# Kernel tuning notes

Measured on AMD Instinct MI355X. Metric: run time of the kernel, lower is better.

The kernel has to match this reference:

```python
import jax, jax.numpy as jnp
import numpy as np

N = 100000          # nodes
E = 1_600_000       # edges (before self loops)
IN = 128            # in_channels
HID = 64            # hidden
HEADS = 4
EPS = 1e-5          # BatchNorm eps
NEG_SLOPE = 0.2     # GATConv leaky_relu slope


def setup_inputs() -> dict:
    key = jax.random.key(0)
    ks = jax.random.split(key, 16)
    he = lambda fan: (2.0 / fan) ** 0.5  # kaiming-normal scale
    d = {
        "x": jax.random.normal(ks[0], (N, IN), jnp.float32),
        "edge_index": jax.random.randint(ks[1], (2, E), 0, N, dtype=jnp.int64),
        "root_index": 0,
        "W1": jax.random.normal(ks[2], (IN, HEADS * HID), jnp.float32) * he(IN),
        "att_src1": jax.random.normal(ks[3], (HEADS, HID), jnp.float32) * 0.1,
        "att_dst1": jax.random.normal(ks[4], (HEADS, HID), jnp.float32) * 0.1,
        "b1": jnp.zeros((HEADS * HID,), jnp.float32),
        "W2": jax.random.normal(ks[5], (HEADS * HID, HID), jnp.float32) * he(HEADS * HID),
        "att_src2": jax.random.normal(ks[6], (1, HID), jnp.float32) * 0.1,
        "att_dst2": jax.random.normal(ks[7], (1, HID), jnp.float32) * 0.1,
        "b2": jnp.zeros((HID,), jnp.float32),
        "bn1_g": jnp.ones((HEADS * HID,), jnp.float32),
        "bn1_b": jnp.zeros((HEADS * HID,), jnp.float32),
        "bn1_m": jnp.zeros((HEADS * HID,), jnp.float32),
        "bn1_v": jnp.ones((HEADS * HID,), jnp.float32),
        "bn2_g": jnp.ones((HID,), jnp.float32),
        "bn2_b": jnp.zeros((HID,), jnp.float32),
        "bn2_m": jnp.zeros((HID,), jnp.float32),
        "bn2_v": jnp.ones((HID,), jnp.float32),
        "cg1_w": jax.random.normal(ks[8], (3 * HID, 64), jnp.float32) * he(3 * HID),
        "cg1_b": jnp.zeros((64,), jnp.float32),
        "cbn_g": jnp.ones((64,), jnp.float32),
        "cbn_b": jnp.zeros((64,), jnp.float32),
        "cbn_m": jnp.zeros((64,), jnp.float32),
        "cbn_v": jnp.ones((64,), jnp.float32),
        "cg2_w": jax.random.normal(ks[9], (64, 32), jnp.float32) * he(64),
        "cg2_b": jnp.zeros((32,), jnp.float32),
        "cg3_w": jax.random.normal(ks[10], (32, 1), jnp.float32) * he(32),
        "cg3_b": jnp.zeros((1,), jnp.float32),
    }
    return d


def _bn_eval(x, g, b, m, v):
    return (x - m) * jax.lax.rsqrt(v + EPS) * g + b


def _gat_conv(x, src, dst, W, att_src, att_dst, bias, heads, out_ch, concat):
    """PyG GATConv (eval mode, self loops already in src/dst)."""
    n = x.shape[0]
    h = (x @ W).reshape(n, heads, out_ch)                # [N,H,C]
    a_src = jnp.einsum('nhc,hc->nh', h, att_src)         # [N,H]
    a_dst = jnp.einsum('nhc,hc->nh', h, att_dst)
    e = jax.nn.leaky_relu(a_src[src] + a_dst[dst], NEG_SLOPE)   # [Etot,H]
    seg_max = jax.ops.segment_max(e, dst, num_segments=n)
    ex = jnp.exp(e - seg_max[dst])
    denom = jax.ops.segment_sum(ex, dst, num_segments=n)
    alpha = ex / (denom[dst] + 1e-16)                    # [Etot,H]
    msg = h[src] * alpha[:, :, None]                     # [Etot,H,C]
    out = jax.ops.segment_sum(msg, dst, num_segments=n)  # [N,H,C]
    if concat:
        return out.reshape(n, heads * out_ch) + bias
    return out.mean(axis=1) + bias


def reference(x, edge_index, root_index, W1, att_src1, att_dst1, b1,
              W2, att_src2, att_dst2, b2,
              bn1_g, bn1_b, bn1_m, bn1_v, bn2_g, bn2_b, bn2_m, bn2_v,
              cg1_w, cg1_b, cbn_g, cbn_b, cbn_m, cbn_v,
              cg2_w, cg2_b, cg3_w, cg3_b):
    n = x.shape[0]
    # add self loops (PyG GATConv default)
    loop = jnp.arange(n, dtype=edge_index.dtype)
    src = jnp.concatenate([edge_index[0], loop])
    dst = jnp.concatenate([edge_index[1], loop])

    h = _gat_conv(x, src, dst, W1, att_src1, att_dst1, b1, HEADS, HID, True)
    h = jax.nn.elu(_bn_eval(h, bn1_g, bn1_b, bn1_m, bn1_v))
    h = _gat_conv(h, src, dst, W2, att_src2, att_dst2, b2, 1, HID, False)
    node_emb = jax.nn.elu(_bn_eval(h, bn2_g, bn2_b, bn2_m, bn2_v))  # [N,HID]

    mean_emb = node_emb.mean(axis=0, keepdims=True)      # [1,HID]
    max_emb = node_emb.max(axis=0, keepdims=True)        # [1,HID]
    safe_root = min(root_index, n - 1)
    root_emb = node_emb[safe_root][None, :]              # single graph path
    g = jnp.concatenate([mean_emb, max_emb, root_emb], axis=-1)  # [1,3*HID]

    g = jax.nn.relu(_bn_eval(g @ cg1_w + cg1_b, cbn_g, cbn_b, cbn_m, cbn_v))
    g = jax.nn.relu(g @ cg2_w + cg2_b)
    logit = (g @ cg3_w + cg3_b).squeeze(-1)              # [1]
    return logit
```

## Files before the change

kernel.cpp:

```cpp
#include <hip/hip_runtime.h>

#define N_NODES 100000
#define N_EDGES 1600000
#define ETOT    1700000
#define IN_CH   128
#define C1      256
#define HID     64
#define BN_EPS  1e-5f
#define SLOPE   0.2f
#define NCHUNK  98
#define FILL_PH 8
#define PH_NODES 12500

typedef __attribute__((ext_vector_type(8))) short s16x8;
typedef __attribute__((ext_vector_type(4))) float f32x4;
#define MFMA16(a, b, c) __builtin_amdgcn_mfma_f32_16x16x32_bf16(a, b, c, 0, 0, 0)

__device__ __forceinline__ float leaky(float x) { return fmaxf(x, SLOPE * x); }
__device__ __forceinline__ float elu_f(float x) { return x > 0.f ? x : __expf(x) - 1.f; }
__device__ __forceinline__ unsigned short f2bf(float f) {
  unsigned int b = __float_as_uint(f);
  return (unsigned short)((b + 0x7FFFu + ((b >> 16) & 1u)) >> 16);
}
__device__ __forceinline__ float bf2f(unsigned short u) {
  return __uint_as_float((unsigned int)u << 16);
}

__global__ void __launch_bounds__(256) k_init_deg(int* __restrict__ deg) {
  int n = blockIdx.x * 256 + threadIdx.x;
  if (n < N_NODES) deg[n] = 1;
}

__global__ void __launch_bounds__(256) k_deg_ph(const int* __restrict__ edge, int* __restrict__ deg) {
  int bpp = (N_EDGES + 1023) >> 10;
  int ph = blockIdx.x / bpp;
  int lo = ph * PH_NODES, hi = lo + PH_NODES;
  int i0 = (blockIdx.x % bpp) * 1024 + threadIdx.x * 4;
  if (i0 >= N_EDGES) return;
  if (i0 + 3 < N_EDGES) {
    int4 dv = *(const int4*)(edge + N_EDGES + i0);
    if (dv.x >= lo && dv.x < hi) atomicAdd(&deg[dv.x], 1);
    if (dv.y >= lo && dv.y < hi) atomicAdd(&deg[dv.y], 1);
    if (dv.z >= lo && dv.z < hi) atomicAdd(&deg[dv.z], 1);
    if (dv.w >= lo && dv.w < hi) atomicAdd(&deg[dv.w], 1);
  } else {
    for (int j = 0; j < 4 && i0 + j < N_EDGES; j++) {
      int d = edge[N_EDGES + i0 + j];
      if (d >= lo && d < hi) atomicAdd(&deg[d], 1);
    }
  }
}

__global__ void __launch_bounds__(256) k_scan_part(const int* __restrict__ deg, int* __restrict__ part) {
  __shared__ int ls[256];
  int t = threadIdx.x;
  int base = blockIdx.x * 1024 + t * 4;
  int s = 0;
#pragma unroll
  for (int j = 0; j < 4; j++) if (base + j < N_NODES) s += deg[base + j];
  ls[t] = s;
  __syncthreads();
  for (int off = 128; off >= 1; off >>= 1) {
    if (t < off) ls[t] += ls[t + off];
    __syncthreads();
  }
  if (t == 0) part[blockIdx.x] = ls[0];
}

__global__ void k_scan_top(int* __restrict__ part, int* __restrict__ row_ptr) {
  if (threadIdx.x == 0 && blockIdx.x == 0) {
    int run = 0;
    for (int i = 0; i < NCHUNK; i++) { int t = part[i]; part[i] = run; run += t; }
    row_ptr[N_NODES] = run;
  }
}

__global__ void __launch_bounds__(256) k_scan_down(const int* __restrict__ deg, const int* __restrict__ part,
                                                   int* __restrict__ row_ptr, int* __restrict__ cursor) {
  __shared__ int ls[256];
  int t = threadIdx.x;
  int base = blockIdx.x * 1024 + t * 4;
  int v[4];
#pragma unroll
  for (int j = 0; j < 4; j++) v[j] = (base + j < N_NODES) ? deg[base + j] : 0;
  int tsum = v[0] + v[1] + v[2] + v[3];
  ls[t] = tsum;
  __syncthreads();
  for (int off = 1; off < 256; off <<= 1) {
    int add = (t >= off) ? ls[t - off] : 0;
    __syncthreads();
    ls[t] += add;
    __syncthreads();
  }
  int excl = ls[t] - tsum + part[blockIdx.x];
#pragma unroll
  for (int j = 0; j < 4; j++) {
    int idx = base + j;
    if (idx < N_NODES) { row_ptr[idx] = excl; cursor[idx] = excl; }
    excl += v[j];
  }
}

__global__ void __launch_bounds__(256) k_fill_ph(const int* __restrict__ edge, int* __restrict__ cursor,
                                                 int* __restrict__ col) {
  int bpp = (ETOT + 255) >> 8;
  int ph = blockIdx.x / bpp;
  int lo = ph * PH_NODES, hi = lo + PH_NODES;
  int i = (blockIdx.x % bpp) * 256 + threadIdx.x;
  if (i >= ETOT) return;
  int d = (i < N_EDGES) ? edge[N_EDGES + i] : (i - N_EDGES);
  if (d < lo || d >= hi) return;
  int s = (i < N_EDGES) ? edge[i] : d;
  int pos = atomicAdd(&cursor[d], 1);
  col[pos] = s;
}

__global__ void __launch_bounds__(256) k_prep(const float* __restrict__ W1, const float* __restrict__ W2,
                                              unsigned short* __restrict__ W1T, unsigned short* __restrict__ W2T) {
  int i = blockIdx.x * 256 + threadIdx.x;
  if (i < IN_CH * C1) {
    int k = i >> 8, c = i & 255;
    W1T[c * IN_CH + k] = f2bf(W1[i]);
  }
  if (i < C1 * HID) {
    int k = i >> 6, c = i & 63;
    W2T[c * C1 + k] = f2bf(W2[i]);
  }
}

__global__ void __launch_bounds__(256) k_gemm1(const float* __restrict__ x, const unsigned short* __restrict__ W1T,
                                               const float* __restrict__ attS, const float* __restrict__ attD,
                                               unsigned short* __restrict__ h1b, float* __restrict__ aS,
                                               float* __restrict__ aD) {
  __shared__ unsigned short As[64][IN_CH + 8];
  int tid = threadIdx.x;
  int w = tid >> 6, lane = tid & 63;
  int l15 = lane & 15, l4 = lane >> 4;
  int row0 = blockIdx.x * 64;
#pragma unroll
  for (int it = 0; it < 8; it++) {
    int idx = tid + it * 256;
    int r = idx >> 5;
    int k4 = (idx & 31) * 4;
    int gr = row0 + r; if (gr >= N_NODES) gr = N_NODES - 1;
    float4 v = *(const float4*)(x + (size_t)gr * IN_CH + k4);
    ushort4 bvec;
    bvec.x = f2bf(v.x); bvec.y = f2bf(v.y); bvec.z = f2bf(v.z); bvec.w = f2bf(v.w);
    *(ushort4*)&As[r][k4] = bvec;
  }
  __syncthreads();
  f32x4 acc[4][4];
#pragma unroll
  for (int mf = 0; mf < 4; mf++)
#pragma unroll
    for (int cf = 0; cf < 4; cf++) acc[mf][cf] = (f32x4){0.f, 0.f, 0.f, 0.f};
#pragma unroll
  for (int ks = 0; ks < 4; ks++) {
    int koff = ks * 32 + l4 * 8;
    s16x8 a[4];
#pragma unroll
    for (int mf = 0; mf < 4; mf++) a[mf] = *(const s16x8*)&As[mf * 16 + l15][koff];
#pragma unroll
    for (int cf = 0; cf < 4; cf++) {
      s16x8 b = *(const s16x8*)(W1T + (size_t)(w * 64 + cf * 16 + l15) * IN_CH + koff);
#pragma unroll
      for (int mf = 0; mf < 4; mf++) acc[mf][cf] = MFMA16(a[mf], b, acc[mf][cf]);
    }
  }
  float as_c[4], ad_c[4];
#pragma unroll
  for (int cf = 0; cf < 4; cf++) {
    as_c[cf] = attS[w * HID + cf * 16 + l15];
    ad_c[cf] = attD[w * HID + cf * 16 + l15];
  }
#pragma unroll
  for (int mf = 0; mf < 4; mf++) {
#pragma unroll
    for (int reg = 0; reg < 4; reg++) {
      int gr = row0 + mf * 16 + l4 * 4 + reg;
      bool ok = gr < N_NODES;
      float s = 0.f, dd = 0.f;
#pragma unroll
      for (int cf = 0; cf < 4; cf++) {
        float v = acc[mf][cf][reg];
        if (ok) h1b[(size_t)gr * C1 + w * 64 + cf * 16 + l15] = f2bf(v);
        s += v * as_c[cf];
        dd += v * ad_c[cf];
      }
#pragma unroll
      for (int m = 1; m <= 8; m <<= 1) { s += __shfl_xor(s, m, 64); dd += __shfl_xor(dd, m, 64); }
      if (ok && l15 == 0) {
        aS[(size_t)gr * 4 + w] = s;
        aD[(size_t)gr * 4 + w] = dd;
      }
    }
  }
}

__global__ void __launch_bounds__(256) k_agg1(const int* __restrict__ row_ptr, const int* __restrict__ col,
                                              const float* __restrict__ aS, const float* __restrict__ aD,
                                              const unsigned short* __restrict__ h1b, const float* __restrict__ b1,
                                              const float* __restrict__ g1, const float* __restrict__ be1,
                                              const float* __restrict__ m1, const float* __restrict__ v1,
                                              unsigned short* __restrict__ hmb) {
  int wave = threadIdx.x >> 6;
  int lane = threadIdx.x & 63;
  int d = blockIdx.x * 4 + wave;
  if (d >= N_NODES) return;
  int head = lane >> 4;
  float ad = aD[d * 4 + head];
  int s0 = row_ptr[d], s1 = row_ptr[d + 1];
  float denom = 0.f;
  float4 acc = {0.f, 0.f, 0.f, 0.f};
  int c0 = lane * 4;
  int i = s0;
  int iend8 = s0 + ((s1 - s0) & ~7);
  for (; i < iend8; i += 8) {
    int cv = col[i + (lane & 7)];
    int sid[8];
#pragma unroll
    for (int j = 0; j < 8; j++) sid[j] = __builtin_amdgcn_readfirstlane(__shfl(cv, j));
    float e[8];
#pragma unroll
    for (int j = 0; j < 8; j++) e[j] = aS[(sid[j] << 2) + head];
    ushort4 h[8];
#pragma unroll
    for (int j = 0; j < 8; j++) h[j] = *(const ushort4*)(h1b + ((size_t)sid[j] << 8) + c0);
    float wv[8];
#pragma unroll
    for (int j = 0; j < 8; j++) wv[j] = __expf(fminf(leaky(e[j] + ad), 80.f));
#pragma unroll
    for (int j = 0; j < 8; j++) {
      denom += wv[j];
      acc.x += wv[j] * bf2f(h[j].x);
      acc.y += wv[j] * bf2f(h[j].y);
      acc.z += wv[j] * bf2f(h[j].z);
      acc.w += wv[j] * bf2f(h[j].w);
    }
  }
  for (; i < s1; i++) {
    int s = __builtin_amdgcn_readfirstlane(col[i]);
    float e = aS[(s << 2) + head];
    ushort4 hv = *(const ushort4*)(h1b + ((size_t)s << 8) + c0);
    float wv = __expf(fminf(leaky(e + ad), 80.f));
    denom += wv;
    acc.x += wv * bf2f(hv.x);
    acc.y += wv * bf2f(hv.y);
    acc.z += wv * bf2f(hv.z);
    acc.w += wv * bf2f(hv.w);
  }
  float inv = 1.f / (denom + 1e-16f);
  float4 bb = *(const float4*)(b1 + c0);
  float4 gg = *(const float4*)(g1 + c0);
  float4 be = *(const float4*)(be1 + c0);
  float4 mm = *(const float4*)(m1 + c0);
  float4 vv = *(const float4*)(v1 + c0);
  ushort4 o;
  o.x = f2bf(elu_f((acc.x * inv + bb.x - mm.x) * rsqrtf(vv.x + BN_EPS) * gg.x + be.x));
  o.y = f2bf(elu_f((acc.y * inv + bb.y - mm.y) * rsqrtf(vv.y + BN_EPS) * gg.y + be.y));
  o.z = f2bf(elu_f((acc.z * inv + bb.z - mm.z) * rsqrtf(vv.z + BN_EPS) * gg.z + be.z));
  o.w = f2bf(elu_f((acc.w * inv + bb.w - mm.w) * rsqrtf(vv.w + BN_EPS) * gg.w + be.w));
  *(ushort4*)(hmb + (size_t)d * C1 + c0) = o;
}

__global__ void __launch_bounds__(256) k_gemm2(const unsigned short* __restrict__ hmb, const unsigned short* __restrict__ W2T,
                                               const float* __restrict__ attS, const float* __restrict__ attD,
                                               unsigned short* __restrict__ h2b, float* __restrict__ aS,
                                               float* __restrict__ aD) {
  __shared__ unsigned short As[64][C1 + 8];
  int tid = threadIdx.x;
  int w = tid >> 6, lane = tid & 63;
  int l15 = lane & 15, l4 = lane >> 4;
  int row0 = blockIdx.x * 64;
#pragma unroll
  for (int it = 0; it < 8; it++) {
    int idx = tid + it * 256;
    int r = idx >> 5;
    int k8 = (idx & 31) * 8;
    int gr = row0 + r; if (gr >= N_NODES) gr = N_NODES - 1;
    *(uint4*)&As[r][k8] = *(const uint4*)(hmb + (size_t)gr * C1 + k8);
  }
  __syncthreads();
  f32x4 acc[4];
#pragma unroll
  for (int cf = 0; cf < 4; cf++) acc[cf] = (f32x4){0.f, 0.f, 0.f, 0.f};
#pragma unroll
  for (int ks = 0; ks < 8; ks++) {
    int koff = ks * 32 + l4 * 8;
    s16x8 a = *(const s16x8*)&As[w * 16 + l15][koff];
#pragma unroll
    for (int cf = 0; cf < 4; cf++) {
      s16x8 b = *(const s16x8*)(W2T + (size_t)(cf * 16 + l15) * C1 + koff);
      acc[cf] = MFMA16(a, b, acc[cf]);
    }
  }
  float as_c[4], ad_c[4];
#pragma unroll
  for (int cf = 0; cf < 4; cf++) {
    as_c[cf] = attS[cf * 16 + l15];
    ad_c[cf] = attD[cf * 16 + l15];
  }
#pragma unroll
  for (int reg = 0; reg < 4; reg++) {
    int gr = row0 + w * 16 + l4 * 4 + reg;
    bool ok = gr < N_NODES;
    float s = 0.f, dd = 0.f;
#pragma unroll
    for (int cf = 0; cf < 4; cf++) {
      float v = acc[cf][reg];
      if (ok) h2b[(size_t)gr * HID + cf * 16 + l15] = f2bf(v);
      s += v * as_c[cf];
      dd += v * ad_c[cf];
    }
#pragma unroll
    for (int m = 1; m <= 8; m <<= 1) { s += __shfl_xor(s, m, 64); dd += __shfl_xor(dd, m, 64); }
    if (ok && l15 == 0) { aS[gr] = s; aD[gr] = dd; }
  }
}

__global__ void __launch_bounds__(256) k_agg2(const int* __restrict__ row_ptr, const int* __restrict__ col,
                                              const float* __restrict__ aS, const float* __restrict__ aD,
                                              const unsigned short* __restrict__ h2b, const float* __restrict__ b2,
                                              const float* __restrict__ g2, const float* __restrict__ be2,
                                              const float* __restrict__ m2, const float* __restrict__ v2,
                                              float* __restrict__ emb) {
  int wave = threadIdx.x >> 6;
  int lane = threadIdx.x & 63;
  int d = blockIdx.x * 4 + wave;
  if (d >= N_NODES) return;
  float ad = aD[d];
  int s0 = row_ptr[d], s1 = row_ptr[d + 1];
  float denom = 0.f, acc = 0.f;
  int i = s0;
  int iend8 = s0 + ((s1 - s0) & ~7);
  for (; i < iend8; i += 8) {
    int cv = col[i + (lane & 7)];
    int sid[8];
#pragma unroll
    for (int j = 0; j < 8; j++) sid[j] = __builtin_amdgcn_readfirstlane(__shfl(cv, j));
    float e[8];
#pragma unroll
    for (int j = 0; j < 8; j++) e[j] = aS[sid[j]];
    unsigned short h[8];
#pragma unroll
    for (int j = 0; j < 8; j++) h[j] = h2b[((size_t)sid[j] << 6) + lane];
    float wv[8];
#pragma unroll
    for (int j = 0; j < 8; j++) wv[j] = __expf(fminf(leaky(e[j] + ad), 80.f));
#pragma unroll
    for (int j = 0; j < 8; j++) {
      denom += wv[j];
      acc += wv[j] * bf2f(h[j]);
    }
  }
  for (; i < s1; i++) {
    int s = __builtin_amdgcn_readfirstlane(col[i]);
    float e = aS[s];
    unsigned short hv = h2b[((size_t)s << 6) + lane];
    float wv = __expf(fminf(leaky(e + ad), 80.f));
    denom += wv;
    acc += wv * bf2f(hv);
  }
  float o = acc / (denom + 1e-16f) + b2[lane];
  o = (o - m2[lane]) * rsqrtf(v2[lane] + BN_EPS) * g2[lane] + be2[lane];
  emb[(size_t)d * HID + lane] = elu_f(o);
}

__global__ void __launch_bounds__(256) k_pool(const float* __restrict__ emb, float* __restrict__ psum,
                                              float* __restrict__ pmax) {
  __shared__ float ss[4][64], sm[4][64];
  int t = threadIdx.x;
  int c = t & 63, rg = t >> 6;
  float s = 0.f, m = -INFINITY;
  for (int n = blockIdx.x * 4 + rg; n < N_NODES; n += gridDim.x * 4) {
    float v = emb[(size_t)n * HID + c];
    s += v; m = fmaxf(m, v);
  }
  ss[rg][c] = s; sm[rg][c] = m;
  __syncthreads();
  if (t < 64) {
    psum[blockIdx.x * 64 + t] = ss[0][t] + ss[1][t] + ss[2][t] + ss[3][t];
    pmax[blockIdx.x * 64 + t] = fmaxf(fmaxf(sm[0][t], sm[1][t]), fmaxf(sm[2][t], sm[3][t]));
  }
}

__global__ void __launch_bounds__(256) k_final(const float* __restrict__ psum, const float* __restrict__ pmax,
                                               const float* __restrict__ emb, const int* __restrict__ rootp,
                                               const float* __restrict__ cg1w, const float* __restrict__ cg1b,
                                               const float* __restrict__ cbng, const float* __restrict__ cbnb,
                                               const float* __restrict__ cbnm, const float* __restrict__ cbnv,
                                               const float* __restrict__ cg2w, const float* __restrict__ cg2b,
                                               const float* __restrict__ cg3w, const float* __restrict__ cg3b,
                                               float* __restrict__ out) {
  __shared__ float ss[4][64], sm[4][64];
  __shared__ float g[192], t1[64], t2[32];
  int t = threadIdx.x;
  int c = t & 63, q = t >> 6;
  float s = 0.f, m = -INFINITY;
  for (int b = q; b < 256; b += 4) {
    s += psum[b * 64 + c];
    m = fmaxf(m, pmax[b * 64 + c]);
  }
  ss[q][c] = s; sm[q][c] = m;
  __syncthreads();
  if (t < 64) {
    float tot = ss[0][t] + ss[1][t] + ss[2][t] + ss[3][t];
    float mx = fmaxf(fmaxf(sm[0][t], sm[1][t]), fmaxf(sm[2][t], sm[3][t]));
    int root = rootp[0];
    if (root > N_NODES - 1) root = N_NODES - 1;
    if (root < 0) root = 0;
    g[t] = tot / (float)N_NODES;
    g[64 + t] = mx;
    g[128 + t] = emb[(size_t)root * HID + t];
  }
  __syncthreads();
  if (t < 64) {
    float o = cg1b[t];
    for (int i = 0; i < 192; i++) o += g[i] * cg1w[i * 64 + t];
    o = (o - cbnm[t]) * rsqrtf(cbnv[t] + BN_EPS) * cbng[t] + cbnb[t];
    t1[t] = o > 0.f ? o : 0.f;
  }
  __syncthreads();
  if (t < 32) {
    float o = cg2b[t];
    for (int i = 0; i < 64; i++) o += t1[i] * cg2w[i * 32 + t];
    t2[t] = o > 0.f ? o : 0.f;
  }
  __syncthreads();
  if (t == 0) {
    float o = cg3b[0];
    for (int i = 0; i < 32; i++) o += t2[i] * cg3w[i];
    out[0] = o;
  }
}

extern "C" void kernel_launch(void* const* d_in, const int* in_sizes, int n_in,
                              void* d_out, int out_size, void* d_ws, size_t ws_size,
                              hipStream_t stream) {
  const float* x     = (const float*)d_in[0];
  const int*   edge  = (const int*)d_in[1];
  const int*   root  = (const int*)d_in[2];
  const float* W1    = (const float*)d_in[3];
  const float* attS1 = (const float*)d_in[4];
  const float* attD1 = (const float*)d_in[5];
  const float* b1    = (const float*)d_in[6];
  const float* W2    = (const float*)d_in[7];
  const float* attS2 = (const float*)d_in[8];
  const float* attD2 = (const float*)d_in[9];
  const float* b2    = (const float*)d_in[10];
  const float* bn1g  = (const float*)d_in[11];
  const float* bn1b  = (const float*)d_in[12];
  const float* bn1m  = (const float*)d_in[13];
  const float* bn1v  = (const float*)d_in[14];
  const float* bn2g  = (const float*)d_in[15];
  const float* bn2b  = (const float*)d_in[16];
  const float* bn2m  = (const float*)d_in[17];
  const float* bn2v  = (const float*)d_in[18];
  const float* cg1w  = (const float*)d_in[19];
  const float* cg1b  = (const float*)d_in[20];
  const float* cbng  = (const float*)d_in[21];
  const float* cbnb  = (const float*)d_in[22];
  const float* cbnm  = (const float*)d_in[23];
  const float* cbnv  = (const float*)d_in[24];
  const float* cg2w  = (const float*)d_in[25];
  const float* cg2b  = (const float*)d_in[26];
  const float* cg3w  = (const float*)d_in[27];
  const float* cg3b  = (const float*)d_in[28];

  char* ws = (char*)d_ws;
  size_t off = 0;
  auto carve = [&](size_t bytes) { char* p = ws + off; off += (bytes + 255) & ~(size_t)255; return p; };
  unsigned short* h1b = (unsigned short*)carve((size_t)N_NODES * C1 * 2);
  unsigned short* hmb = (unsigned short*)carve((size_t)N_NODES * C1 * 2);
  float* aS1     = (float*)carve((size_t)N_NODES * 4 * 4);
  float* aD1     = (float*)carve((size_t)N_NODES * 4 * 4);
  int*   deg     = (int*)  carve((size_t)N_NODES * 4);
  int*   row_ptr = (int*)  carve((size_t)(N_NODES + 1) * 4);
  int*   cursor  = (int*)  carve((size_t)N_NODES * 4);
  int*   col     = (int*)  carve((size_t)ETOT * 4);
  int*   part    = (int*)  carve(512);
  unsigned short* W1T = (unsigned short*)carve((size_t)IN_CH * C1 * 2);
  unsigned short* W2T = (unsigned short*)carve((size_t)C1 * HID * 2);
  unsigned short* h2b = h1b;
  float* aS2  = (float*)(h1b + (size_t)N_NODES * HID);
  float* aD2  = aS2 + N_NODES;
  float* emb  = (float*)hmb;
  float* psum = emb + (size_t)N_NODES * HID;
  float* pmax = psum + 256 * 64;

  int bpp_deg  = (N_EDGES + 1023) >> 10;
  int bpp_fill = (ETOT + 255) >> 8;
  k_init_deg<<<(N_NODES + 255) / 256, 256, 0, stream>>>(deg);
  k_deg_ph<<<bpp_deg * FILL_PH, 256, 0, stream>>>(edge, deg);
  k_prep<<<(IN_CH * C1 + 255) / 256, 256, 0, stream>>>(W1, W2, W1T, W2T);
  k_scan_part<<<NCHUNK, 256, 0, stream>>>(deg, part);
  k_scan_top<<<1, 64, 0, stream>>>(part, row_ptr);
  k_scan_down<<<NCHUNK, 256, 0, stream>>>(deg, part, row_ptr, cursor);
  k_fill_ph<<<bpp_fill * FILL_PH, 256, 0, stream>>>(edge, cursor, col);
  k_gemm1<<<(N_NODES + 63) / 64, 256, 0, stream>>>(x, W1T, attS1, attD1, h1b, aS1, aD1);
  k_agg1<<<(N_NODES + 3) / 4, 256, 0, stream>>>(row_ptr, col, aS1, aD1, h1b, b1, bn1g, bn1b, bn1m, bn1v, hmb);
  k_gemm2<<<(N_NODES + 63) / 64, 256, 0, stream>>>(hmb, W2T, attS2, attD2, h2b, aS2, aD2);
  k_agg2<<<(N_NODES + 3) / 4, 256, 0, stream>>>(row_ptr, col, aS2, aD2, h2b, b2, bn2g, bn2b, bn2m, bn2v, emb);
  k_pool<<<256, 256, 0, stream>>>(emb, psum, pmax);
  k_final<<<1, 256, 0, stream>>>(psum, pmax, emb, root, cg1w, cg1b, cbng, cbnb, cbnm, cbnv,
                                 cg2w, cg2b, cg3w, cg3b, (float*)d_out);
}
```

Before: 502.9 us.

## Precompute per-edge attention weights during CSR fill and in separate layer-2 pass

Moves GEMM1 ahead of the CSR fill so the fill kernel can compute the layer-1 exp(leaky) attention weights per edge (all four heads) and store them in CSR order along with each edge's destination. A new kernel computes the layer-2 edge weights from col and edst. The aggregation kernels then read the weights contiguously instead of gathering aS by source and running exp inline. In exchange it writes and reads an extra ETOT*16-byte weight array plus ETOT*4 bytes each for edst and w2, and adds one kernel launch.

```diff
diff --git a/kernel.cpp b/kernel.cpp
--- a/kernel.cpp
+++ b/kernel.cpp
@@ -102,7 +102,9 @@
 }
 
 __global__ void __launch_bounds__(256) k_fill_ph(const int* __restrict__ edge, int* __restrict__ cursor,
-                                                 int* __restrict__ col) {
+                                                 const float* __restrict__ aS, const float* __restrict__ aD,
+                                                 int* __restrict__ col, int* __restrict__ edst,
+                                                 float* __restrict__ w1) {
   int bpp = (ETOT + 255) >> 8;
   int ph = blockIdx.x / bpp;
   int lo = ph * PH_NODES, hi = lo + PH_NODES;
@@ -113,6 +115,23 @@
   int s = (i < N_EDGES) ? edge[i] : d;
   int pos = atomicAdd(&cursor[d], 1);
   col[pos] = s;
+  edst[pos] = d;
+  float4 as4 = *(const float4*)(aS + (size_t)s * 4);
+  float4 ad4 = *(const float4*)(aD + (size_t)d * 4);
+  float4 w;
+  w.x = __expf(fminf(leaky(as4.x + ad4.x), 80.f));
+  w.y = __expf(fminf(leaky(as4.y + ad4.y), 80.f));
+  w.z = __expf(fminf(leaky(as4.z + ad4.z), 80.f));
+  w.w = __expf(fminf(leaky(as4.w + ad4.w), 80.f));
+  *(float4*)(w1 + (size_t)pos * 4) = w;
+}
+
+__global__ void __launch_bounds__(256) k_w2(const int* __restrict__ col, const int* __restrict__ edst,
+                                            const float* __restrict__ aS, const float* __restrict__ aD,
+                                            float* __restrict__ w2) {
+  int i = blockIdx.x * 256 + threadIdx.x;
+  if (i >= ETOT) return;
+  w2[i] = __expf(fminf(leaky(aS[col[i]] + aD[edst[i]]), 80.f));
 }
 
 __global__ void __launch_bounds__(256) k_prep(const float* __restrict__ W1, const float* __restrict__ W2,
@@ -198,7 +217,7 @@
 }
 
 __global__ void __launch_bounds__(256) k_agg1(const int* __restrict__ row_ptr, const int* __restrict__ col,
-                                              const float* __restrict__ aS, const float* __restrict__ aD,
+                                              const float* __restrict__ w1,
                                               const unsigned short* __restrict__ h1b, const float* __restrict__ b1,
                                               const float* __restrict__ g1, const float* __restrict__ be1,
                                               const float* __restrict__ m1, const float* __restrict__ v1,
@@ -208,7 +227,6 @@
   int d = blockIdx.x * 4 + wave;
   if (d >= N_NODES) return;
   int head = lane >> 4;
-  float ad = aD[d * 4 + head];
   int s0 = row_ptr[d], s1 = row_ptr[d + 1];
   float denom = 0.f;
   float4 acc = {0.f, 0.f, 0.f, 0.f};
@@ -220,15 +238,12 @@
     int sid[8];
 #pragma unroll
     for (int j = 0; j < 8; j++) sid[j] = __builtin_amdgcn_readfirstlane(__shfl(cv, j));
-    float e[8];
-#pragma unroll
-    for (int j = 0; j < 8; j++) e[j] = aS[(sid[j] << 2) + head];
+    float wv[8];
+#pragma unroll
+    for (int j = 0; j < 8; j++) wv[j] = w1[(size_t)(i + j) * 4 + head];
     ushort4 h[8];
 #pragma unroll
     for (int j = 0; j < 8; j++) h[j] = *(const ushort4*)(h1b + ((size_t)sid[j] << 8) + c0);
-    float wv[8];
-#pragma unroll
-    for (int j = 0; j < 8; j++) wv[j] = __expf(fminf(leaky(e[j] + ad), 80.f));
 #pragma unroll
     for (int j = 0; j < 8; j++) {
       denom += wv[j];
@@ -240,9 +255,8 @@
   }
   for (; i < s1; i++) {
     int s = __builtin_amdgcn_readfirstlane(col[i]);
-    float e = aS[(s << 2) + head];
+    float wv = w1[(size_t)i * 4 + head];
     ushort4 hv = *(const ushort4*)(h1b + ((size_t)s << 8) + c0);
-    float wv = __expf(fminf(leaky(e + ad), 80.f));
     denom += wv;
     acc.x += wv * bf2f(hv.x);
     acc.y += wv * bf2f(hv.y);
@@ -319,7 +333,7 @@
 }
 
 __global__ void __launch_bounds__(256) k_agg2(const int* __restrict__ row_ptr, const int* __restrict__ col,
-                                              const float* __restrict__ aS, const float* __restrict__ aD,
+                                              const float* __restrict__ w2,
                                               const unsigned short* __restrict__ h2b, const float* __restrict__ b2,
                                               const float* __restrict__ g2, const float* __restrict__ be2,
                                               const float* __restrict__ m2, const float* __restrict__ v2,
@@ -328,7 +342,6 @@
   int lane = threadIdx.x & 63;
   int d = blockIdx.x * 4 + wave;
   if (d >= N_NODES) return;
-  float ad = aD[d];
   int s0 = row_ptr[d], s1 = row_ptr[d + 1];
   float denom = 0.f, acc = 0.f;
   int i = s0;
@@ -338,15 +351,12 @@
     int sid[8];
 #pragma unroll
     for (int j = 0; j < 8; j++) sid[j] = __builtin_amdgcn_readfirstlane(__shfl(cv, j));
-    float e[8];
-#pragma unroll
-    for (int j = 0; j < 8; j++) e[j] = aS[sid[j]];
+    float wv[8];
+#pragma unroll
+    for (int j = 0; j < 8; j++) wv[j] = w2[i + j];
     unsigned short h[8];
 #pragma unroll
     for (int j = 0; j < 8; j++) h[j] = h2b[((size_t)sid[j] << 6) + lane];
-    float wv[8];
-#pragma unroll
-    for (int j = 0; j < 8; j++) wv[j] = __expf(fminf(leaky(e[j] + ad), 80.f));
 #pragma unroll
     for (int j = 0; j < 8; j++) {
       denom += wv[j];
@@ -355,9 +365,8 @@
   }
   for (; i < s1; i++) {
     int s = __builtin_amdgcn_readfirstlane(col[i]);
-    float e = aS[s];
+    float wv = w2[i];
     unsigned short hv = h2b[((size_t)s << 6) + lane];
-    float wv = __expf(fminf(leaky(e + ad), 80.f));
     denom += wv;
     acc += wv * bf2f(hv);
   }
@@ -478,12 +487,15 @@
   int*   row_ptr = (int*)  carve((size_t)(N_NODES + 1) * 4);
   int*   cursor  = (int*)  carve((size_t)N_NODES * 4);
   int*   col     = (int*)  carve((size_t)ETOT * 4);
+  int*   edst    = (int*)  carve((size_t)ETOT * 4);
+  float* w1      = (float*)carve((size_t)ETOT * 4 * 4);
   int*   part    = (int*)  carve(512);
   unsigned short* W1T = (unsigned short*)carve((size_t)IN_CH * C1 * 2);
   unsigned short* W2T = (unsigned short*)carve((size_t)C1 * HID * 2);
   unsigned short* h2b = h1b;
   float* aS2  = (float*)(h1b + (size_t)N_NODES * HID);
   float* aD2  = aS2 + N_NODES;
+  float* w2   = w1;
   float* emb  = (float*)hmb;
   float* psum = emb + (size_t)N_NODES * HID;
   float* pmax = psum + 256 * 64;
@@ -493,14 +505,15 @@
   k_init_deg<<<(N_NODES + 255) / 256, 256, 0, stream>>>(deg);
   k_deg_ph<<<bpp_deg * FILL_PH, 256, 0, stream>>>(edge, deg);
   k_prep<<<(IN_CH * C1 + 255) / 256, 256, 0, stream>>>(W1, W2, W1T, W2T);
+  k_gemm1<<<(N_NODES + 63) / 64, 256, 0, stream>>>(x, W1T, attS1, attD1, h1b, aS1, aD1);
   k_scan_part<<<NCHUNK, 256, 0, stream>>>(deg, part);
   k_scan_top<<<1, 64, 0, stream>>>(part, row_ptr);
   k_scan_down<<<NCHUNK, 256, 0, stream>>>(deg, part, row_ptr, cursor);
-  k_fill_ph<<<bpp_fill * FILL_PH, 256, 0, stream>>>(edge, cursor, col);
-  k_gemm1<<<(N_NODES + 63) / 64, 256, 0, stream>>>(x, W1T, attS1, attD1, h1b, aS1, aD1);
-  k_agg1<<<(N_NODES + 3) / 4, 256, 0, stream>>>(row_ptr, col, aS1, aD1, h1b, b1, bn1g, bn1b, bn1m, bn1v, hmb);
+  k_fill_ph<<<bpp_fill * FILL_PH, 256, 0, stream>>>(edge, cursor, aS1, aD1, col, edst, w1);
+  k_agg1<<<(N_NODES + 3) / 4, 256, 0, stream>>>(row_ptr, col, w1, h1b, b1, bn1g, bn1b, bn1m, bn1v, hmb);
   k_gemm2<<<(N_NODES + 63) / 64, 256, 0, stream>>>(hmb, W2T, attS2, attD2, h2b, aS2, aD2);
-  k_agg2<<<(N_NODES + 3) / 4, 256, 0, stream>>>(row_ptr, col, aS2, aD2, h2b, b2, bn2g, bn2b, bn2m, bn2v, emb);
+  k_w2<<<(ETOT + 255) / 256, 256, 0, stream>>>(col, edst, aS2, aD2, w2);
+  k_agg2<<<(N_NODES + 3) / 4, 256, 0, stream>>>(row_ptr, col, w2, h2b, b2, bn2g, bn2b, bn2m, bn2v, emb);
   k_pool<<<256, 256, 0, stream>>>(emb, psum, pmax);
   k_final<<<1, 256, 0, stream>>>(psum, pmax, emb, root, cg1w, cg1b, cbng, cbnb, cbnm, cbnv,
                                  cg2w, cg2b, cg3w, cg3b, (float*)d_out);
```

After: 517.8 us. 3.0% more time.
